# Kernel tuning notes

Hardware: AMD Instinct MI355X
Metric: run time of the kernel (lower is better)

## Reference

```python
import jax, jax.numpy as jnp
import numpy as np

N_NODES = 100000
N_EDGES = 1600000
IN_FT = 128
OUT_FT = 128


def gcn_conv(x, W, b, src, dst, n):
    """PyG-style GCNConv: add self-loops, symmetric normalization, linear."""
    h = x @ W  # [n, out]
    loop = jnp.arange(n, dtype=src.dtype)
    s = jnp.concatenate([src, loop])  # sources (x_j)
    d = jnp.concatenate([dst, loop])  # targets (aggregation index)
    deg = jax.ops.segment_sum(jnp.ones(s.shape[0], dtype=h.dtype), d, num_segments=n)
    dinv = jnp.where(deg > 0, jax.lax.rsqrt(deg), 0.0)
    norm = dinv[s] * dinv[d]  # [E+n]
    msg = h[s] * norm[:, None]  # gather + scale
    out = jax.ops.segment_sum(msg, d, num_segments=n)  # scatter-add
    return out + b


def setup_inputs() -> dict:
    key = jax.random.key(0)
    ks = jax.random.split(key, 12)
    def lin(kw, kb, fan_in, fan_out):
        bound = 1.0 / np.sqrt(fan_in)
        W = jax.random.uniform(kw, (fan_in, fan_out), jnp.float32, -bound, bound)
        b = jax.random.uniform(kb, (fan_out,), jnp.float32, -bound, bound)
        return W, b
    x = jax.random.normal(ks[0], (N_NODES, IN_FT), jnp.float32)
    edge_index = jax.random.randint(ks[1], (2, N_EDGES), 0, N_NODES, jnp.int64)
    proj_W, proj_b = lin(ks[2], ks[3], IN_FT, OUT_FT)
    W1, b1 = lin(ks[4], ks[5], IN_FT, OUT_FT)
    W2, b2 = lin(ks[6], ks[7], 2 * OUT_FT, OUT_FT)
    W3, b3 = lin(ks[8], ks[9], 3 * OUT_FT, OUT_FT)
    return {"x": x, "edge_index": edge_index, "proj_W": proj_W, "proj_b": proj_b,
            "W1": W1, "b1": b1, "W2": W2, "b2": b2, "W3": W3, "b3": b3}


def reference(x, edge_index, proj_W, proj_b, W1, b1, W2, b2, W3, b3):
    n = x.shape[0]
    src, dst = edge_index[0], edge_index[1]
    act = jax.nn.relu
    x_p = act(x @ proj_W + proj_b)
    h1 = act(gcn_conv(x, W1, b1, src, dst, n))
    in2 = jnp.concatenate([x_p, h1], axis=1)
    h2 = act(gcn_conv(in2, W2, b2, src, dst, n))
    in3 = jnp.concatenate([x_p, h1, h2], axis=1)
    h3 = act(gcn_conv(in3, W3, b3, src, dst, n))
    return h3
```

## Files before the change

### kernel.cpp

```cpp
#include <hip/hip_runtime.h>

#define N_NODES 100000
#define N_EDGES 1600000

typedef __attribute__((ext_vector_type(8))) short bf16x8;
typedef __attribute__((ext_vector_type(4))) float f32x4;
typedef __attribute__((ext_vector_type(2))) float f32x2;
typedef __attribute__((ext_vector_type(4))) unsigned short u16x4;

__device__ __forceinline__ float b2f(unsigned short u) {
    union { unsigned int i; float f; } v; v.i = ((unsigned int)u) << 16; return v.f;
}
__device__ __forceinline__ unsigned short f2b(float f) {
    union { float ff; unsigned int i; } v; v.ff = f;
    unsigned int x = v.i;
    x += 0x7fffu + ((x >> 16) & 1u);
    return (unsigned short)(x >> 16);
}

__global__ __launch_bounds__(256) void k_cast4(const float* __restrict__ in,
                                               unsigned short* __restrict__ out, int n4) {
    int i = blockIdx.x * 256 + threadIdx.x;
    if (i < n4) {
        f32x4 v = *(const f32x4*)&in[(size_t)i * 4];
        u16x4 o;
        o[0] = f2b(v[0]); o[1] = f2b(v[1]); o[2] = f2b(v[2]); o[3] = f2b(v[3]);
        *(u16x4*)&out[(size_t)i * 4] = o;
    }
}

__global__ __launch_bounds__(256) void k_castWT(
    const float* __restrict__ pW, const float* __restrict__ W1,
    const float* __restrict__ W2, const float* __restrict__ W3,
    unsigned short* __restrict__ out)
{
    int i = blockIdx.x * 256 + threadIdx.x;
    if (i >= 114688) return;
    const float* src; int K, base;
    if (i < 16384)      { src = pW; K = 128; base = 0; }
    else if (i < 32768) { src = W1; K = 128; base = 16384; }
    else if (i < 65536) { src = W2; K = 256; base = 32768; }
    else                { src = W3; K = 384; base = 65536; }
    int loc = i - base;
    int col = loc / K, k = loc - col * K;
    out[i] = f2b(src[(size_t)k * 128 + col]);
}

#define NB1 8
#define WIN1 ((N_NODES + NB1 - 1) / NB1)
#define CAP1 204800
#define PART_BLOCKS 782
#define PART_EPB 2048
#define SUBS 32
#define NWIN (NB1 * SUBS)
#define WIN2 ((WIN1 + SUBS - 1) / SUBS)
#define CAP2 8192
#define PART2_BLOCKS 2048

__global__ void k_init(int* gcur, int* gcur2) {
    int i = threadIdx.x;
    if (i < NB1)  gcur[i]  = i * CAP1;
    if (i < NWIN) gcur2[i] = i * CAP2;
}

__global__ __launch_bounds__(256) void k_part(
    const int* __restrict__ src, const int* __restrict__ dst,
    int* __restrict__ gcur, unsigned long long* __restrict__ part)
{
    __shared__ int bcnt[NB1];
    __shared__ int lcur[NB1];
    const int tid = threadIdx.x;
    const int ll  = tid & 63;
    const int base = blockIdx.x * PART_EPB;
    int sv[8], dv[8], bv[8];
    int mycnt[NB1] = {0, 0, 0, 0, 0, 0, 0, 0};
#pragma unroll
    for (int u = 0; u < 8; ++u) {
        int e = base + u * 256 + tid;
        bool val = e < N_EDGES;
        sv[u] = val ? src[e] : 0;
        dv[u] = val ? dst[e] : 0;
        bv[u] = val ? dv[u] / WIN1 : -1;
#pragma unroll
        for (int bk = 0; bk < NB1; ++bk) mycnt[bk] += (bv[u] == bk);
    }
    if (tid < NB1) bcnt[tid] = 0;
    __syncthreads();
#pragma unroll
    for (int bk = 0; bk < NB1; ++bk) {
        int c = mycnt[bk];
        for (int o = 1; o < 64; o <<= 1) c += __shfl_xor(c, o, 64);
        if (ll == 0 && c) atomicAdd(&bcnt[bk], c);
    }
    __syncthreads();
    if (tid < NB1) lcur[tid] = atomicAdd(&gcur[tid], bcnt[tid]);
    __syncthreads();
#pragma unroll
    for (int u = 0; u < 8; ++u) {
        unsigned long long masks[NB1]; int cnts[NB1];
#pragma unroll
        for (int bk = 0; bk < NB1; ++bk) {
            masks[bk] = __ballot(bv[u] == bk);
            cnts[bk]  = __popcll(masks[bk]);
        }
        int posv = 0;
        if (ll < NB1) posv = atomicAdd(&lcur[ll], cnts[ll]);
        int myoff = 0;
#pragma unroll
        for (int bk = 0; bk < NB1; ++bk) {
            int bb = __builtin_amdgcn_readlane(posv, bk);
            if (bv[u] == bk) myoff = bb + __popcll(masks[bk] & ((1ULL << ll) - 1ULL));
        }
        if (bv[u] >= 0)
            part[myoff] = ((unsigned long long)(unsigned)dv[u] << 32) | (unsigned)sv[u];
    }
}

__global__ __launch_bounds__(256) void k_part2(
    const unsigned long long* __restrict__ part, const int* __restrict__ gcur,
    int* __restrict__ gcur2, unsigned long long* __restrict__ part2)
{
    __shared__ int bcnt[SUBS];
    __shared__ int lcur[SUBS];
    const int w   = blockIdx.x & (NB1 - 1);
    const int g   = blockIdx.x >> 3;
    const int tid = threadIdx.x;
    const int b0  = w * CAP1;
    const int cnt = gcur[w] - b0;
    const int chunk = (cnt + 255) >> 8;
    const int lo = g * chunk;
    const int hi = min(lo + chunk, cnt);
    const int rounds = (hi > lo) ? ((hi - lo + 255) >> 8) : 0;
    const int nlo_base = w * WIN1;

    unsigned long long ev[4];
    int bkv[4];
    if (tid < SUBS) bcnt[tid] = 0;
    __syncthreads();
    for (int r = 0; r < rounds; ++r) {
        int i = lo + r * 256 + tid;
        bool val = i < hi;
        unsigned long long e = val ? part[b0 + i] : 0ULL;
        int bk = val ? ((int)(e >> 32) - nlo_base) / WIN2 : -1;
        ev[r] = e; bkv[r] = bk;
        if (val) atomicAdd(&bcnt[bk], 1);
    }
    __syncthreads();
    if (tid < SUBS) lcur[tid] = atomicAdd(&gcur2[w * SUBS + tid], bcnt[tid]);
    __syncthreads();
    for (int r = 0; r < rounds; ++r) {
        int mybk = bkv[r];
        if (mybk >= 0) {
            int off = atomicAdd(&lcur[mybk], 1);
            part2[off] = ev[r];
        }
    }
}

__global__ __launch_bounds__(512) void k_histw(
    const unsigned long long* __restrict__ part2, const int* __restrict__ gcur2,
    int* __restrict__ deg)
{
    __shared__ int cnt[WIN2];
    const int q = blockIdx.x;
    const int w = q >> 5, s = q & (SUBS - 1);
    const int nlo = w * WIN1 + s * WIN2;
    const int nhi = w * WIN1 + min((s + 1) * WIN2, WIN1);
    const int wn = nhi - nlo;
    for (int i = threadIdx.x; i < wn; i += 512) cnt[i] = 0;
    __syncthreads();
    const int b0 = q * CAP2;
    const int ec = gcur2[q] - b0;
    for (int i = threadIdx.x; i < ec; i += 512) {
        int d = (int)(part2[b0 + i] >> 32);
        atomicAdd(&cnt[d - nlo], 1);
    }
    __syncthreads();
    for (int i = threadIdx.x; i < wn; i += 512) deg[nlo + i] = cnt[i] + 1;
}

#define SCAN_CHUNK 2048
#define SCAN_BLOCKS ((N_NODES + SCAN_CHUNK - 1) / SCAN_CHUNK)

__global__ __launch_bounds__(256) void k_deg_part(const int* __restrict__ deg,
                                                  int* __restrict__ psum) {
    int b = blockIdx.x, t = threadIdx.x;
    int base = b * SCAN_CHUNK + t * 8;
    int s = 0;
#pragma unroll
    for (int i = 0; i < 8; ++i) { int idx = base + i; if (idx < N_NODES) s += deg[idx]; }
    for (int o = 1; o < 64; o <<= 1) s += __shfl_xor(s, o, 64);
    __shared__ int ws[4];
    if ((t & 63) == 0) ws[t >> 6] = s;
    __syncthreads();
    if (t == 0) psum[b] = ws[0] + ws[1] + ws[2] + ws[3];
}

__global__ void k_scan_off(const int* __restrict__ psum, int* __restrict__ poff) {
    int t = threadIdx.x;
    int v = (t < SCAN_BLOCKS) ? psum[t] : 0;
    int sc = v;
    for (int o = 1; o < 64; o <<= 1) { int u = __shfl_up(sc, o, 64); if (t >= o) sc += u; }
    if (t < SCAN_BLOCKS) poff[t] = sc - v;
}

__global__ __launch_bounds__(256) void k_scan_final(
    const int* __restrict__ deg, const int* __restrict__ poff,
    int* __restrict__ row_ptr, float* __restrict__ dinv)
{
    int b = blockIdx.x, t = threadIdx.x;
    int base = b * SCAN_CHUNK + t * 8;
    int v[8]; int s = 0;
#pragma unroll
    for (int i = 0; i < 8; ++i) { int idx = base + i; v[i] = (idx < N_NODES) ? deg[idx] : 0; s += v[i]; }
    int lane = t & 63, wv = t >> 6;
    int sc = s;
    for (int o = 1; o < 64; o <<= 1) { int u = __shfl_up(sc, o, 64); if (lane >= o) sc += u; }
    __shared__ int wsum[4];
    if (lane == 63) wsum[wv] = sc;
    __syncthreads();
    int woff = 0;
    for (int i = 0; i < wv; ++i) woff += wsum[i];
    int excl = poff[b] + woff + sc - s;
#pragma unroll
    for (int i = 0; i < 8; ++i) {
        int idx = base + i;
        if (idx < N_NODES) {
            row_ptr[idx] = excl;
            dinv[idx] = rsqrtf((float)v[i]);
            excl += v[i];
        }
    }
}

__global__ __launch_bounds__(512) void k_sortw(
    const unsigned long long* __restrict__ part2, const int* __restrict__ gcur2,
    const int* __restrict__ row_ptr, int* __restrict__ ssrc)
{
    __shared__ int cur[WIN2];
    const int q = blockIdx.x;
    const int w = q >> 5, s = q & (SUBS - 1);
    const int nlo = w * WIN1 + s * WIN2;
    const int nhi = w * WIN1 + min((s + 1) * WIN2, WIN1);
    const int wn = nhi - nlo;
    for (int i = threadIdx.x; i < wn; i += 512) cur[i] = row_ptr[nlo + i];
    __syncthreads();
    const int b0 = q * CAP2;
    const int ec = gcur2[q] - b0;
    for (int i = threadIdx.x; i < ec; i += 512) {
        unsigned long long e = part2[b0 + i];
        int d = (int)(e >> 32);
        int p = atomicAdd(&cur[d - nlo], 1);
        ssrc[p] = (int)(e & 0xffffffffu);
    }
}

template<int NC, bool RELU, bool BIAS, bool SCALE>
__global__ __launch_bounds__(256) void k_gemm(
    const unsigned short* __restrict__ A0, const unsigned short* __restrict__ A1,
    const unsigned short* __restrict__ A2, const unsigned short* __restrict__ WtG,
    const float* __restrict__ bias, const float* __restrict__ dinv,
    unsigned short* __restrict__ out)
{
    const int tid  = threadIdx.x;
    const int wave = tid >> 6, lane = tid & 63;
    const int l15 = lane & 15, lg = lane >> 4;
    const int K = NC * 128;
    const int rbase = blockIdx.x * 128 + wave * 32;

    f32x4 acc[2][8];
#pragma unroll
    for (int i = 0; i < 2; ++i)
#pragma unroll
        for (int j = 0; j < 8; ++j) acc[i][j] = (f32x4)(0.0f);

    int ar0 = rbase + l15;      if (ar0 >= N_NODES) ar0 = N_NODES - 1;
    int ar1 = rbase + 16 + l15; if (ar1 >= N_NODES) ar1 = N_NODES - 1;

    for (int c = 0; c < NC; ++c) {
        const unsigned short* Ac = (c == 0) ? A0 : ((c == 1) ? A1 : A2);
#pragma unroll
        for (int ks = 0; ks < 4; ++ks) {
            const int ko = ks * 32 + lg * 8;
            bf16x8 a0 = *(const bf16x8*)&Ac[(size_t)ar0 * 128 + ko];
            bf16x8 a1 = *(const bf16x8*)&Ac[(size_t)ar1 * 128 + ko];
#pragma unroll
            for (int cf = 0; cf < 8; ++cf) {
                bf16x8 b = *(const bf16x8*)&WtG[(size_t)(cf * 16 + l15) * K + c * 128 + ko];
                acc[0][cf] = __builtin_amdgcn_mfma_f32_16x16x32_bf16(a0, b, acc[0][cf], 0, 0, 0);
                acc[1][cf] = __builtin_amdgcn_mfma_f32_16x16x32_bf16(a1, b, acc[1][cf], 0, 0, 0);
            }
        }
    }
    float bvs[8];
#pragma unroll
    for (int cf = 0; cf < 8; ++cf) bvs[cf] = BIAS ? bias[cf * 16 + l15] : 0.0f;
#pragma unroll
    for (int ai = 0; ai < 2; ++ai) {
#pragma unroll
        for (int j = 0; j < 4; ++j) {
            int row = rbase + ai * 16 + lg * 4 + j;
            if (row < N_NODES) {
                float sc = SCALE ? dinv[row] : 1.0f;
#pragma unroll
                for (int cf = 0; cf < 8; ++cf) {
                    float v = acc[ai][cf][j] + bvs[cf];
                    if (RELU)  v = fmaxf(v, 0.0f);
                    if (SCALE) v *= sc;
                    out[(size_t)row * 128 + cf * 16 + l15] = f2b(v);
                }
            }
        }
    }
}

template<bool FINAL>
__global__ __launch_bounds__(256) void k_agg(
    const unsigned short* __restrict__ t, const int* __restrict__ ssrc,
    const int* __restrict__ row_ptr, const int* __restrict__ deg,
    const float* __restrict__ dinv, const float* __restrict__ bias,
    void* __restrict__ out_v)
{
    const int wave = threadIdx.x >> 6;
    const int lane = threadIdx.x & 63;
    const int node = blockIdx.x * 4 + wave;
    if (node >= N_NODES) return;

    const int beg = row_ptr[node];
    const int cnt = deg[node] - 1;
    float a0 = 0.0f, a1 = 0.0f;

    for (int kb = 0; kb < cnt; kb += 64) {
        const int rem = cnt - kb;
        const int lim = rem < 64 ? rem : 64;
        int sk = 0;
        if (lane < lim) sk = ssrc[beg + kb + lane];

        int k = 0;
        for (; k + 8 <= lim; k += 8) {
            unsigned int p[8];
#pragma unroll
            for (int u = 0; u < 8; ++u) {
                int s = __builtin_amdgcn_readlane(sk, k + u);
                p[u] = *(const unsigned int*)&t[(size_t)s * 128 + lane * 2];
            }
#pragma unroll
            for (int u = 0; u < 8; ++u) {
                a0 += b2f((unsigned short)(p[u] & 0xffffu));
                a1 += b2f((unsigned short)(p[u] >> 16));
            }
        }
        for (; k < lim; ++k) {
            int s0 = __builtin_amdgcn_readlane(sk, k);
            unsigned int p0 = *(const unsigned int*)&t[(size_t)s0 * 128 + lane * 2];
            a0 += b2f((unsigned short)(p0 & 0xffffu));
            a1 += b2f((unsigned short)(p0 >> 16));
        }
    }

    unsigned int ps = *(const unsigned int*)&t[(size_t)node * 128 + lane * 2];
    a0 += b2f((unsigned short)(ps & 0xffffu));
    a1 += b2f((unsigned short)(ps >> 16));

    float di = dinv[node];
    f32x2 bv = *(const f32x2*)&bias[lane * 2];
    float o0 = fmaxf(di * a0 + bv[0], 0.0f);
    float o1 = fmaxf(di * a1 + bv[1], 0.0f);
    if (FINAL) {
        f32x2 po; po[0] = o0; po[1] = o1;
        *(f32x2*)((float*)out_v + (size_t)node * 128 + lane * 2) = po;
    } else {
        unsigned short* out = (unsigned short*)out_v;
        unsigned int po = (unsigned int)f2b(o0) | ((unsigned int)f2b(o1) << 16);
        *(unsigned int*)&out[(size_t)node * 128 + lane * 2] = po;
    }
}

extern "C" void kernel_launch(void* const* d_in, const int* in_sizes, int n_in,
                              void* d_out, int out_size, void* d_ws, size_t ws_size,
                              hipStream_t stream)
{
    const float* x  = (const float*)d_in[0];
    const int*   ei = (const int*)d_in[1];
    const float* pW = (const float*)d_in[2];
    const float* pb = (const float*)d_in[3];
    const float* W1 = (const float*)d_in[4];
    const float* b1 = (const float*)d_in[5];
    const float* W2 = (const float*)d_in[6];
    const float* b2 = (const float*)d_in[7];
    const float* W3 = (const float*)d_in[8];
    const float* b3 = (const float*)d_in[9];
    const int* src = ei;
    const int* dst = ei + N_EDGES;

    char* ws = (char*)d_ws;
    size_t off = 0;
    auto alloc = [&](size_t bytes) -> char* {
        char* p = ws + off; off += (bytes + 255) & ~(size_t)255; return p;
    };
    const size_t NB = (size_t)N_NODES * 128;
    unsigned short* xb = (unsigned short*)alloc(NB * 2);
    unsigned short* xp = (unsigned short*)alloc(NB * 2);
    unsigned short* h1 = (unsigned short*)alloc(NB * 2);
    unsigned short* h2 = (unsigned short*)alloc(NB * 2);
    unsigned short* tb = (unsigned short*)alloc(NB * 2);
    unsigned short* Wb = (unsigned short*)alloc((size_t)114688 * 2);
    int*   deg  = (int*)alloc((size_t)N_NODES * 4);
    int*   rp   = (int*)alloc((size_t)N_NODES * 4);
    float* dinv = (float*)alloc((size_t)N_NODES * 4);
    int*   psum = (int*)alloc((size_t)SCAN_BLOCKS * 4);
    int*   poff = (int*)alloc((size_t)SCAN_BLOCKS * 4);
    int*   gcur = (int*)alloc((size_t)NB1 * 4);
    int*   gcur2= (int*)alloc((size_t)NWIN * 4);
    int*   ssrc = (int*)alloc((size_t)(N_EDGES + N_NODES) * 4);

    unsigned long long* part  = (unsigned long long*)tb;
    unsigned long long* part2 = (unsigned long long*)h2;

    unsigned short* pWt = Wb;
    unsigned short* W1t = Wb + 16384;
    unsigned short* W2t = Wb + 32768;
    unsigned short* W3t = Wb + 65536;

    k_cast4<<<(int)(NB / 4 + 255) / 256, 256, 0, stream>>>(x, xb, (int)(NB / 4));
    k_castWT<<<(114688 + 255) / 256, 256, 0, stream>>>(pW, W1, W2, W3, Wb);

    k_init<<<1, 512, 0, stream>>>(gcur, gcur2);
    k_part<<<PART_BLOCKS, 256, 0, stream>>>(src, dst, gcur, part);
    k_part2<<<PART2_BLOCKS, 256, 0, stream>>>(part, gcur, gcur2, part2);
    k_histw<<<NWIN, 512, 0, stream>>>(part2, gcur2, deg);
    k_deg_part<<<SCAN_BLOCKS, 256, 0, stream>>>(deg, psum);
    k_scan_off<<<1, 64, 0, stream>>>(psum, poff);
    k_scan_final<<<SCAN_BLOCKS, 256, 0, stream>>>(deg, poff, rp, dinv);
    k_sortw<<<NWIN, 512, 0, stream>>>(part2, gcur2, rp, ssrc);

    const int gblocks = (N_NODES + 127) / 128;
    const int ablocks = (N_NODES + 3) / 4;

    k_gemm<1, true,  true,  false><<<gblocks, 256, 0, stream>>>(xb, nullptr, nullptr, pWt, pb, dinv, xp);
    k_gemm<1, false, false, true ><<<gblocks, 256, 0, stream>>>(xb, nullptr, nullptr, W1t, nullptr, dinv, tb);
    k_agg<false><<<ablocks, 256, 0, stream>>>(tb, ssrc, rp, deg, dinv, b1, h1);
    k_gemm<2, false, false, true ><<<gblocks, 256, 0, stream>>>(xp, h1, nullptr, W2t, nullptr, dinv, tb);
    k_agg<false><<<ablocks, 256, 0, stream>>>(tb, ssrc, rp, deg, dinv, b2, h2);
    k_gemm<3, false, false, true ><<<gblocks, 256, 0, stream>>>(xp, h1, h2, W3t, nullptr, dinv, tb);
    k_agg<true><<<ablocks, 256, 0, stream>>>(tb, ssrc, rp, deg, dinv, b3, d_out);
}
```

Measured before the change: 548.3 us.

## Fuse prep casts, fold degree scan into sort, merge first two GEMMs

The x cast, weight transpose-cast and cursor init now run in a single prep kernel. The three-kernel degree scan is replaced by a 256-thread scan over per-window totals (edge count plus node count from gcur2), and each sort block then scans its own window to write row_ptr and dinv. The projection GEMM and the W1 GEMM share one pass over x with two accumulator sets. The aim is fewer launches and one fewer read of x, at the cost of more registers in the dual GEMM and smaller 64-row tiles.

```diff
diff --git a/kernel.cpp b/kernel.cpp
--- a/kernel.cpp
+++ b/kernel.cpp
@@ -16,34 +16,6 @@
     unsigned int x = v.i;
     x += 0x7fffu + ((x >> 16) & 1u);
     return (unsigned short)(x >> 16);
-}
-
-__global__ __launch_bounds__(256) void k_cast4(const float* __restrict__ in,
-                                               unsigned short* __restrict__ out, int n4) {
-    int i = blockIdx.x * 256 + threadIdx.x;
-    if (i < n4) {
-        f32x4 v = *(const f32x4*)&in[(size_t)i * 4];
-        u16x4 o;
-        o[0] = f2b(v[0]); o[1] = f2b(v[1]); o[2] = f2b(v[2]); o[3] = f2b(v[3]);
-        *(u16x4*)&out[(size_t)i * 4] = o;
-    }
-}
-
-__global__ __launch_bounds__(256) void k_castWT(
-    const float* __restrict__ pW, const float* __restrict__ W1,
-    const float* __restrict__ W2, const float* __restrict__ W3,
-    unsigned short* __restrict__ out)
-{
-    int i = blockIdx.x * 256 + threadIdx.x;
-    if (i >= 114688) return;
-    const float* src; int K, base;
-    if (i < 16384)      { src = pW; K = 128; base = 0; }
-    else if (i < 32768) { src = W1; K = 128; base = 16384; }
-    else if (i < 65536) { src = W2; K = 256; base = 32768; }
-    else                { src = W3; K = 384; base = 65536; }
-    int loc = i - base;
-    int col = loc / K, k = loc - col * K;
-    out[i] = f2b(src[(size_t)k * 128 + col]);
 }
 
 #define NB1 8
@@ -57,10 +29,39 @@
 #define CAP2 8192
 #define PART2_BLOCKS 2048
 
-__global__ void k_init(int* gcur, int* gcur2) {
-    int i = threadIdx.x;
-    if (i < NB1)  gcur[i]  = i * CAP1;
-    if (i < NWIN) gcur2[i] = i * CAP2;
+#define NQX 3200000
+#define NWEL 114688
+
+__global__ __launch_bounds__(256) void k_prep(
+    const float* __restrict__ x,
+    const float* __restrict__ pW, const float* __restrict__ W1,
+    const float* __restrict__ W2, const float* __restrict__ W3,
+    unsigned short* __restrict__ xb, unsigned short* __restrict__ Wb,
+    int* __restrict__ gcur, int* __restrict__ gcur2)
+{
+    int i = blockIdx.x * 256 + threadIdx.x;
+    if (i < NQX) {
+        f32x4 v = *(const f32x4*)&x[(size_t)i * 4];
+        u16x4 o;
+        o[0] = f2b(v[0]); o[1] = f2b(v[1]); o[2] = f2b(v[2]); o[3] = f2b(v[3]);
+        *(u16x4*)&xb[(size_t)i * 4] = o;
+        return;
+    }
+    int j = i - NQX;
+    if (j < NWEL) {
+        const float* src; int K, base;
+        if (j < 16384)      { src = pW; K = 128; base = 0; }
+        else if (j < 32768) { src = W1; K = 128; base = 16384; }
+        else if (j < 65536) { src = W2; K = 256; base = 32768; }
+        else                { src = W3; K = 384; base = 65536; }
+        int loc = j - base;
+        int col = loc / K, k = loc - col * K;
+        Wb[j] = f2b(src[(size_t)k * 128 + col]);
+        return;
+    }
+    int k = j - NWEL;
+    if (k < NB1) gcur[k] = k * CAP1;
+    else if (k < NB1 + NWIN) gcur2[k - NB1] = (k - NB1) * CAP2;
 }
 
 __global__ __launch_bounds__(256) void k_part(
@@ -179,75 +180,55 @@
     for (int i = threadIdx.x; i < wn; i += 512) deg[nlo + i] = cnt[i] + 1;
 }
 
-#define SCAN_CHUNK 2048
-#define SCAN_BLOCKS ((N_NODES + SCAN_CHUNK - 1) / SCAN_CHUNK)
-
-__global__ __launch_bounds__(256) void k_deg_part(const int* __restrict__ deg,
-                                                  int* __restrict__ psum) {
-    int b = blockIdx.x, t = threadIdx.x;
-    int base = b * SCAN_CHUNK + t * 8;
-    int s = 0;
-#pragma unroll
-    for (int i = 0; i < 8; ++i) { int idx = base + i; if (idx < N_NODES) s += deg[idx]; }
-    for (int o = 1; o < 64; o <<= 1) s += __shfl_xor(s, o, 64);
-    __shared__ int ws[4];
-    if ((t & 63) == 0) ws[t >> 6] = s;
-    __syncthreads();
-    if (t == 0) psum[b] = ws[0] + ws[1] + ws[2] + ws[3];
-}
-
-__global__ void k_scan_off(const int* __restrict__ psum, int* __restrict__ poff) {
-    int t = threadIdx.x;
-    int v = (t < SCAN_BLOCKS) ? psum[t] : 0;
+__global__ void k_scan_off(const int* __restrict__ gcur2, int* __restrict__ poff) {
+    __shared__ int wsum[4];
+    const int q = threadIdx.x;
+    const int s = q & (SUBS - 1);
+    const int wn = min((s + 1) * WIN2, WIN1) - s * WIN2;
+    int v = (gcur2[q] - q * CAP2) + wn;
+    int lane = q & 63, wv = q >> 6;
     int sc = v;
-    for (int o = 1; o < 64; o <<= 1) { int u = __shfl_up(sc, o, 64); if (t >= o) sc += u; }
-    if (t < SCAN_BLOCKS) poff[t] = sc - v;
-}
-
-__global__ __launch_bounds__(256) void k_scan_final(
-    const int* __restrict__ deg, const int* __restrict__ poff,
-    int* __restrict__ row_ptr, float* __restrict__ dinv)
-{
-    int b = blockIdx.x, t = threadIdx.x;
-    int base = b * SCAN_CHUNK + t * 8;
-    int v[8]; int s = 0;
-#pragma unroll
-    for (int i = 0; i < 8; ++i) { int idx = base + i; v[i] = (idx < N_NODES) ? deg[idx] : 0; s += v[i]; }
-    int lane = t & 63, wv = t >> 6;
-    int sc = s;
     for (int o = 1; o < 64; o <<= 1) { int u = __shfl_up(sc, o, 64); if (lane >= o) sc += u; }
-    __shared__ int wsum[4];
     if (lane == 63) wsum[wv] = sc;
     __syncthreads();
     int woff = 0;
     for (int i = 0; i < wv; ++i) woff += wsum[i];
-    int excl = poff[b] + woff + sc - s;
-#pragma unroll
-    for (int i = 0; i < 8; ++i) {
-        int idx = base + i;
-        if (idx < N_NODES) {
-            row_ptr[idx] = excl;
-            dinv[idx] = rsqrtf((float)v[i]);
-            excl += v[i];
-        }
-    }
+    poff[q] = woff + sc - v;
 }
 
 __global__ __launch_bounds__(512) void k_sortw(
     const unsigned long long* __restrict__ part2, const int* __restrict__ gcur2,
-    const int* __restrict__ row_ptr, int* __restrict__ ssrc)
+    const int* __restrict__ poff, const int* __restrict__ deg,
+    int* __restrict__ row_ptr, float* __restrict__ dinv, int* __restrict__ ssrc)
 {
     __shared__ int cur[WIN2];
+    __shared__ int wsum[8];
     const int q = blockIdx.x;
     const int w = q >> 5, s = q & (SUBS - 1);
     const int nlo = w * WIN1 + s * WIN2;
     const int nhi = w * WIN1 + min((s + 1) * WIN2, WIN1);
     const int wn = nhi - nlo;
-    for (int i = threadIdx.x; i < wn; i += 512) cur[i] = row_ptr[nlo + i];
-    __syncthreads();
+    const int tid = threadIdx.x;
+
+    int v = (tid < wn) ? deg[nlo + tid] : 0;
+    int lane = tid & 63, wv = tid >> 6;
+    int sc = v;
+    for (int o = 1; o < 64; o <<= 1) { int u = __shfl_up(sc, o, 64); if (lane >= o) sc += u; }
+    if (lane == 63) wsum[wv] = sc;
+    __syncthreads();
+    int woff = 0;
+    for (int i = 0; i < wv; ++i) woff += wsum[i];
+    int rp = poff[q] + woff + sc - v;
+    if (tid < wn) {
+        row_ptr[nlo + tid] = rp;
+        dinv[nlo + tid] = rsqrtf((float)v);
+        cur[tid] = rp;
+    }
+    __syncthreads();
+
     const int b0 = q * CAP2;
     const int ec = gcur2[q] - b0;
-    for (int i = threadIdx.x; i < ec; i += 512) {
+    for (int i = tid; i < ec; i += 512) {
         unsigned long long e = part2[b0 + i];
         int d = (int)(e >> 32);
         int p = atomicAdd(&cur[d - nlo], 1);
@@ -255,12 +236,56 @@
     }
 }
 
-template<int NC, bool RELU, bool BIAS, bool SCALE>
+__global__ __launch_bounds__(256) void k_gemm_dual(
+    const unsigned short* __restrict__ xb, const unsigned short* __restrict__ pWt,
+    const unsigned short* __restrict__ W1t, const float* __restrict__ pb,
+    const float* __restrict__ dinv, unsigned short* __restrict__ xp,
+    unsigned short* __restrict__ tb)
+{
+    const int tid  = threadIdx.x;
+    const int wave = tid >> 6, lane = tid & 63;
+    const int l15 = lane & 15, lg = lane >> 4;
+    const int rbase = blockIdx.x * 64 + wave * 16;
+
+    f32x4 accP[8], acc1[8];
+#pragma unroll
+    for (int i = 0; i < 8; ++i) { accP[i] = (f32x4)(0.0f); acc1[i] = (f32x4)(0.0f); }
+
+    int arow = rbase + l15; if (arow >= N_NODES) arow = N_NODES - 1;
+
+#pragma unroll
+    for (int ks = 0; ks < 4; ++ks) {
+        const int ko = ks * 32 + lg * 8;
+        bf16x8 a = *(const bf16x8*)&xb[(size_t)arow * 128 + ko];
+#pragma unroll
+        for (int cf = 0; cf < 8; ++cf) {
+            bf16x8 bP = *(const bf16x8*)&pWt[(size_t)(cf * 16 + l15) * 128 + ko];
+            bf16x8 b1 = *(const bf16x8*)&W1t[(size_t)(cf * 16 + l15) * 128 + ko];
+            accP[cf] = __builtin_amdgcn_mfma_f32_16x16x32_bf16(a, bP, accP[cf], 0, 0, 0);
+            acc1[cf] = __builtin_amdgcn_mfma_f32_16x16x32_bf16(a, b1, acc1[cf], 0, 0, 0);
+        }
+    }
+#pragma unroll
+    for (int cf = 0; cf < 8; ++cf) {
+        int col = cf * 16 + l15;
+        float bv = pb[col];
+#pragma unroll
+        for (int j = 0; j < 4; ++j) {
+            int row = rbase + lg * 4 + j;
+            if (row < N_NODES) {
+                float sc = dinv[row];
+                xp[(size_t)row * 128 + col] = f2b(fmaxf(accP[cf][j] + bv, 0.0f));
+                tb[(size_t)row * 128 + col] = f2b(acc1[cf][j] * sc);
+            }
+        }
+    }
+}
+
+template<int NC>
 __global__ __launch_bounds__(256) void k_gemm(
     const unsigned short* __restrict__ A0, const unsigned short* __restrict__ A1,
     const unsigned short* __restrict__ A2, const unsigned short* __restrict__ WtG,
-    const float* __restrict__ bias, const float* __restrict__ dinv,
-    unsigned short* __restrict__ out)
+    const float* __restrict__ dinv, unsigned short* __restrict__ out)
 {
     const int tid  = threadIdx.x;
     const int wave = tid >> 6, lane = tid & 63;
@@ -292,23 +317,16 @@
             }
         }
     }
-    float bvs[8];
-#pragma unroll
-    for (int cf = 0; cf < 8; ++cf) bvs[cf] = BIAS ? bias[cf * 16 + l15] : 0.0f;
 #pragma unroll
     for (int ai = 0; ai < 2; ++ai) {
 #pragma unroll
         for (int j = 0; j < 4; ++j) {
             int row = rbase + ai * 16 + lg * 4 + j;
             if (row < N_NODES) {
-                float sc = SCALE ? dinv[row] : 1.0f;
-#pragma unroll
-                for (int cf = 0; cf < 8; ++cf) {
-                    float v = acc[ai][cf][j] + bvs[cf];
-                    if (RELU)  v = fmaxf(v, 0.0f);
-                    if (SCALE) v *= sc;
-                    out[(size_t)row * 128 + cf * 16 + l15] = f2b(v);
-                }
+                float sc = dinv[row];
+#pragma unroll
+                for (int cf = 0; cf < 8; ++cf)
+                    out[(size_t)row * 128 + cf * 16 + l15] = f2b(acc[ai][cf][j] * sc);
             }
         }
     }
@@ -404,12 +422,11 @@
     unsigned short* h1 = (unsigned short*)alloc(NB * 2);
     unsigned short* h2 = (unsigned short*)alloc(NB * 2);
     unsigned short* tb = (unsigned short*)alloc(NB * 2);
-    unsigned short* Wb = (unsigned short*)alloc((size_t)114688 * 2);
+    unsigned short* Wb = (unsigned short*)alloc((size_t)NWEL * 2);
     int*   deg  = (int*)alloc((size_t)N_NODES * 4);
     int*   rp   = (int*)alloc((size_t)N_NODES * 4);
     float* dinv = (float*)alloc((size_t)N_NODES * 4);
-    int*   psum = (int*)alloc((size_t)SCAN_BLOCKS * 4);
-    int*   poff = (int*)alloc((size_t)SCAN_BLOCKS * 4);
+    int*   poff = (int*)alloc((size_t)NWIN * 4);
     int*   gcur = (int*)alloc((size_t)NB1 * 4);
     int*   gcur2= (int*)alloc((size_t)NWIN * 4);
     int*   ssrc = (int*)alloc((size_t)(N_EDGES + N_NODES) * 4);
@@ -422,26 +439,22 @@
     unsigned short* W2t = Wb + 32768;
     unsigned short* W3t = Wb + 65536;
 
-    k_cast4<<<(int)(NB / 4 + 255) / 256, 256, 0, stream>>>(x, xb, (int)(NB / 4));
-    k_castWT<<<(114688 + 255) / 256, 256, 0, stream>>>(pW, W1, W2, W3, Wb);
-
-    k_init<<<1, 512, 0, stream>>>(gcur, gcur2);
+    const int prep_blocks = (NQX + NWEL + NB1 + NWIN + 255) / 256;
+    k_prep<<<prep_blocks, 256, 0, stream>>>(x, pW, W1, W2, W3, xb, Wb, gcur, gcur2);
     k_part<<<PART_BLOCKS, 256, 0, stream>>>(src, dst, gcur, part);
     k_part2<<<PART2_BLOCKS, 256, 0, stream>>>(part, gcur, gcur2, part2);
     k_histw<<<NWIN, 512, 0, stream>>>(part2, gcur2, deg);
-    k_deg_part<<<SCAN_BLOCKS, 256, 0, stream>>>(deg, psum);
-    k_scan_off<<<1, 64, 0, stream>>>(psum, poff);
-    k_scan_final<<<SCAN_BLOCKS, 256, 0, stream>>>(deg, poff, rp, dinv);
-    k_sortw<<<NWIN, 512, 0, stream>>>(part2, gcur2, rp, ssrc);
-
+    k_scan_off<<<1, 256, 0, stream>>>(gcur2, poff);
+    k_sortw<<<NWIN, 512, 0, stream>>>(part2, gcur2, poff, deg, rp, dinv, ssrc);
+
+    const int dblocks = (N_NODES + 63) / 64;
     const int gblocks = (N_NODES + 127) / 128;
     const int ablocks = (N_NODES + 3) / 4;
 
-    k_gemm<1, true,  true,  false><<<gblocks, 256, 0, stream>>>(xb, nullptr, nullptr, pWt, pb, dinv, xp);
-    k_gemm<1, false, false, true ><<<gblocks, 256, 0, stream>>>(xb, nullptr, nullptr, W1t, nullptr, dinv, tb);
+    k_gemm_dual<<<dblocks, 256, 0, stream>>>(xb, pWt, W1t, pb, dinv, xp, tb);
     k_agg<false><<<ablocks, 256, 0, stream>>>(tb, ssrc, rp, deg, dinv, b1, h1);
-    k_gemm<2, false, false, true ><<<gblocks, 256, 0, stream>>>(xp, h1, nullptr, W2t, nullptr, dinv, tb);
+    k_gemm<2><<<gblocks, 256, 0, stream>>>(xp, h1, nullptr, W2t, dinv, tb);
     k_agg<false><<<ablocks, 256, 0, stream>>>(tb, ssrc, rp, deg, dinv, b2, h2);
-    k_gemm<3, false, false, true ><<<gblocks, 256, 0, stream>>>(xp, h1, h2, W3t, nullptr, dinv, tb);
+    k_gemm<3><<<gblocks, 256, 0, stream>>>(xp, h1, h2, W3t, dinv, tb);
     k_agg<true><<<ablocks, 256, 0, stream>>>(tb, ssrc, rp, deg, dinv, b3, d_out);
 }
```

Measured after the change: 553.4 us. No clear change (+0.9%).
